# Kernel optimization log

Hardware: AMD Instinct MI355X
Metric: run time of the kernel (lower is better)

The kernel has to match this reference:

```python
import jax, jax.numpy as jnp
import numpy as np

D = 128      # hidden_dim
B = 256      # num graphs in batch
NH = 6144    # head-drug nodes
NT = 6144    # tail-drug nodes
EH = 10240   # head line-graph nodes (edges)
ET = 10240   # tail line-graph nodes (edges)


def _even_batch(n, b):
    # sorted graph assignment with every segment non-empty (PyG Batch invariant)
    return (jnp.arange(n) * b // n).astype(jnp.int32)


def setup_inputs() -> dict:
    key = jax.random.key(0)
    ks = jax.random.split(key, 12)
    w = lambda k: jax.random.normal(k, (D, D), dtype=jnp.float32) * 0.05
    bb = lambda k: jax.random.normal(k, (D,), dtype=jnp.float32) * 0.05
    return {
        "x_node_h": jax.random.normal(ks[0], (NH, D), dtype=jnp.float32),
        "x_node_t": jax.random.normal(ks[1], (NT, D), dtype=jnp.float32),
        "x_line_h": jax.random.normal(ks[2], (EH, D), dtype=jnp.float32),
        "x_line_t": jax.random.normal(ks[3], (ET, D), dtype=jnp.float32),
        "Wh_w": w(ks[4]), "Wh_b": bb(ks[5]),
        "Wt_w": w(ks[6]), "Wt_b": bb(ks[7]),
        "Whl_w": w(ks[8]), "Whl_b": bb(ks[9]),
        "Wtl_w": w(ks[10]), "Wtl_b": bb(ks[11]),
        "h_batch": _even_batch(NH, B),
        "t_batch": _even_batch(NT, B),
        "h_ebatch": _even_batch(EH, B),
        "t_ebatch": _even_batch(ET, B),
        "num_graphs": B,
    }


def _seg_softmax(v, seg, num_segments):
    m = jax.ops.segment_max(v, seg, num_segments=num_segments)
    e = jnp.exp(v - m[seg])
    s = jax.ops.segment_sum(e, seg, num_segments=num_segments)
    return e / s[seg]


def _seg_count(seg, num_segments, dtype):
    c = jax.ops.segment_sum(jnp.ones_like(seg, dtype=dtype), seg, num_segments=num_segments)
    return jnp.maximum(c, 1)


def _mutual_attn(xh, xt, Wh_w, Wh_b, Wt_w, Wt_b, bh, bt, num_graphs):
    lin = lambda x, W, b: x @ W.T + b
    xh1 = lin(xh, Wh_w, Wh_b)
    xt1 = lin(xt, Wt_w, Wt_b)
    xt2 = lin(xt, Wh_w, Wh_b)
    xh2 = lin(xh, Wt_w, Wt_b)
    # (x_t2 @ x_h2^T)^T == x_h2 @ x_t2^T
    alpha = jnp.tanh(xh1 @ xt1.T + xh2 @ xt2.T)  # [Nh, Nt]
    cnt_h = _seg_count(bh, num_graphs, alpha.dtype)
    cnt_t = _seg_count(bt, num_graphs, alpha.dtype)
    # global_mean_pool over rows, then diag of [t_batch]-gather == per-column gather
    pooled_rows = jax.ops.segment_sum(alpha, bh, num_segments=num_graphs) / cnt_h[:, None]  # [B, Nt]
    b_t = pooled_rows[bt, jnp.arange(xt.shape[0])]  # [Nt]
    p_t = _seg_softmax(b_t, bt, num_graphs)
    s_t = jax.ops.segment_sum(p_t[:, None] * xt, bt, num_segments=num_graphs)  # [B, D]
    pooled_cols = jax.ops.segment_sum(alpha.T, bt, num_segments=num_graphs) / cnt_t[:, None]  # [B, Nh]
    b_h = pooled_cols[bh, jnp.arange(xh.shape[0])]  # [Nh]
    p_h = _seg_softmax(b_h, bh, num_graphs)
    s_h = jax.ops.segment_sum(p_h[:, None] * xh, bh, num_segments=num_graphs)  # [B, D]
    return s_h, s_t


def reference(x_node_h, x_node_t, x_line_h, x_line_t,
              Wh_w, Wh_b, Wt_w, Wt_b, Whl_w, Whl_b, Wtl_w, Wtl_b,
              h_batch, t_batch, h_ebatch, t_ebatch, num_graphs):
    s_h, s_t = _mutual_attn(x_node_h, x_node_t, Wh_w, Wh_b, Wt_w, Wt_b,
                            h_batch, t_batch, num_graphs)
    s_h_line, s_t_line = _mutual_attn(x_line_h, x_line_t, Whl_w, Whl_b, Wtl_w, Wtl_b,
                                      h_ebatch, t_ebatch, num_graphs)
    return (s_h, s_t, s_h_line, s_t_line)
```

## Files before the change

### kernel.cpp

```cpp
#include <hip/hip_runtime.h>
#include <math.h>

#define D 128

typedef float f32x4 __attribute__((ext_vector_type(4)));
typedef _Float16 f16x8 __attribute__((ext_vector_type(8)));

union PK4 { _Float16 h[4]; ushort4 v; };

__device__ __forceinline__ f16x8 cvt8(float4 a, float4 b) {
    f16x8 r;
    r[0] = (_Float16)a.x; r[1] = (_Float16)a.y; r[2] = (_Float16)a.z; r[3] = (_Float16)a.w;
    r[4] = (_Float16)b.x; r[5] = (_Float16)b.y; r[6] = (_Float16)b.z; r[7] = (_Float16)b.w;
    return r;
}

__device__ __forceinline__ float tanh_fast(float x) {
    float cx = fminf(fmaxf(x, -15.f), 15.f);
    float t = __expf(2.f * cx);
    return __fdividef(t - 1.f, t + 1.f);
}

template <int LEVEL>
__device__ __forceinline__ void body(
    int g, const float* __restrict__ xh, const float* __restrict__ xt,
    const float* __restrict__ WH, const float* __restrict__ WT,
    const float* __restrict__ bH, const float* __restrict__ bT,
    float* __restrict__ osh, float* __restrict__ ost,
    _Float16* GH, _Float16* GT, _Float16* XH, _Float16* XT,
    float* colpart, float* bh_s, float* pt_s, float* ph_s)
{
    constexpr int R = LEVEL ? 40 : 24;
    constexpr int TM = LEVEL ? 3 : 2;
    constexpr int PAD = TM * 16;
    constexpr float invR = 1.f / (float)R;

    const int tid = threadIdx.x;
    const int w = tid >> 6, l = tid & 63;
    const int lm = l & 15, lq = l >> 4;
    const int base = g * R;
    const int tile0 = 2 * w;

    f16x8 wf[4][4];
#pragma unroll
    for (int ks = 0; ks < 4; ++ks) {
        const int k0 = ks * 32 + lq * 8;
#pragma unroll
        for (int t = 0; t < 2; ++t) {
            const float* p1 = WH + ((tile0 + t) * 16 + lm) * D + k0;
            wf[t][ks] = cvt8(*reinterpret_cast<const float4*>(p1),
                             *reinterpret_cast<const float4*>(p1 + 4));
            const float* p2 = WT + ((tile0 + t) * 16 + lm) * D + k0;
            wf[2 + t][ks] = cvt8(*reinterpret_cast<const float4*>(p2),
                                 *reinterpret_cast<const float4*>(p2 + 4));
        }
    }

    {
        constexpr int UNITS = 2 * PAD * 32;
        for (int u = tid; u < UNITS; u += 256) {
            const int arr = (u >= PAD * 32);
            const int rem = arr ? (u - PAD * 32) : u;
            const int r = rem >> 5, c4 = rem & 31;
            _Float16* Xs = arr ? XT : XH;
            PK4 pk;
            if (r < R) {
                const float* xs = arr ? xt : xh;
                float4 v = *reinterpret_cast<const float4*>(&xs[(base + r) * D + c4 * 4]);
                pk.h[0] = (_Float16)v.x; pk.h[1] = (_Float16)v.y;
                pk.h[2] = (_Float16)v.z; pk.h[3] = (_Float16)v.w;
            } else {
                pk.v = make_ushort4(0, 0, 0, 0);
            }
            *reinterpret_cast<ushort4*>(&Xs[r * 128 + ((c4 * 4) ^ ((r & 7) << 3))]) = pk.v;
        }
        constexpr int GZ = 2 * (PAD - R) * 64;
        for (int u = tid; u < GZ; u += 256) {
            const int arr = (u >= (PAD - R) * 64);
            const int rem = arr ? (u - (PAD - R) * 64) : u;
            const int r = R + (rem >> 6), c4 = rem & 63;
            _Float16* Gs = arr ? GT : GH;
            *reinterpret_cast<ushort4*>(&Gs[r * 256 + c4 * 4]) = make_ushort4(0, 0, 0, 0);
        }
    }
    __syncthreads();

#pragma unroll
    for (int side = 0; side < 2; ++side) {
        const _Float16* Xs = side ? XT : XH;
        const float* __restrict__ bA = side ? bT : bH;
        const float* __restrict__ bB = side ? bH : bT;
        _Float16* Gs = side ? GT : GH;

        f32x4 acc[TM][4];
#pragma unroll
        for (int ti = 0; ti < TM; ++ti)
#pragma unroll
            for (int c2 = 0; c2 < 4; ++c2) acc[ti][c2] = (f32x4){0.f, 0.f, 0.f, 0.f};

#pragma unroll
        for (int ks = 0; ks < 4; ++ks) {
            const int k0 = ks * 32 + lq * 8;
            const int kx = k0 ^ ((lm & 7) << 3);
            f16x8 q[TM];
#pragma unroll
            for (int ti = 0; ti < TM; ++ti)
                q[ti] = *reinterpret_cast<const f16x8*>(&Xs[(ti * 16 + lm) * 128 + kx]);
#pragma unroll
            for (int c2 = 0; c2 < 4; ++c2) {
                const int wfidx = side ? (c2 ^ 2) : c2;
#pragma unroll
                for (int ti = 0; ti < TM; ++ti)
                    acc[ti][c2] = __builtin_amdgcn_mfma_f32_16x16x32_f16(
                        wf[wfidx][ks], q[ti], acc[ti][c2], 0, 0, 0);
            }
        }

#pragma unroll
        for (int c2 = 0; c2 < 4; ++c2) {
            const int ctl = (c2 < 2) ? (tile0 + c2) : (8 + tile0 + (c2 - 2));
            const int nc = ctl * 16 + lq * 4;
            const float* bp = (ctl < 8) ? (bA + nc) : (bB + nc - 128);
            float4 b4 = *reinterpret_cast<const float4*>(bp);
#pragma unroll
            for (int ti = 0; ti < TM; ++ti) {
                int i = ti * 16 + lm;
                if (i < R) {
                    PK4 pk;
                    pk.h[0] = (_Float16)(acc[ti][c2][0] + b4.x);
                    pk.h[1] = (_Float16)(acc[ti][c2][1] + b4.y);
                    pk.h[2] = (_Float16)(acc[ti][c2][2] + b4.z);
                    pk.h[3] = (_Float16)(acc[ti][c2][3] + b4.w);
                    *reinterpret_cast<ushort4*>(&Gs[i * 256 + (nc ^ ((i & 7) << 3))]) = pk.v;
                }
            }
        }
    }
    __syncthreads();

    float cs[3] = {0.f, 0.f, 0.f};
    if (w < TM) {
        f32x4 acc2[TM];
#pragma unroll
        for (int tj = 0; tj < TM; ++tj) acc2[tj] = (f32x4){0.f, 0.f, 0.f, 0.f};

        const int ri = w * 16 + lm;
#pragma unroll
        for (int ksa = 0; ksa < 8; ++ksa) {
            const int k0 = ksa * 32 + lq * 8;
            const int kx = k0 ^ ((lm & 7) << 3);
            f16x8 A = *reinterpret_cast<const f16x8*>(&GH[ri * 256 + kx]);
#pragma unroll
            for (int tj = 0; tj < TM; ++tj) {
                f16x8 B = *reinterpret_cast<const f16x8*>(&GT[(tj * 16 + lm) * 256 + kx]);
                acc2[tj] = __builtin_amdgcn_mfma_f32_16x16x32_f16(A, B, acc2[tj], 0, 0, 0);
            }
        }

        float at[TM][4];
#pragma unroll
        for (int tj = 0; tj < TM; ++tj)
#pragma unroll
            for (int r = 0; r < 4; ++r) at[tj][r] = tanh_fast(acc2[tj][r]);

#pragma unroll
        for (int r = 0; r < 4; ++r) {
            float s = 0.f;
#pragma unroll
            for (int tj = 0; tj < TM; ++tj) s += at[tj][r];
            s += __shfl_xor(s, 1, 64);
            s += __shfl_xor(s, 2, 64);
            s += __shfl_xor(s, 4, 64);
            s += __shfl_xor(s, 8, 64);
            if (lm == 0) bh_s[w * 16 + lq * 4 + r] = s;
        }
#pragma unroll
        for (int tj = 0; tj < TM; ++tj) {
            float s = 0.f;
#pragma unroll
            for (int r = 0; r < 4; ++r) s += at[tj][r];
            s += __shfl_xor(s, 16, 64);
            s += __shfl_xor(s, 32, 64);
            cs[tj] = s;
        }
    }
#pragma unroll
    for (int tj = 0; tj < 3; ++tj)
        if (lq == 0) colpart[w * 48 + tj * 16 + lm] = (tj < TM) ? cs[tj] : 0.f;
    __syncthreads();

    if (w == 0) {
        float v = (l < 48) ? (colpart[l] + colpart[48 + l] + colpart[96 + l] + colpart[144 + l]) : 0.f;
        float val = (l < R) ? v * invR : -INFINITY;
        float m = val;
        for (int o = 32; o; o >>= 1) m = fmaxf(m, __shfl_xor(m, o, 64));
        float e = (l < R) ? __expf(val - m) : 0.f;
        float s = e;
        for (int o = 32; o; o >>= 1) s += __shfl_xor(s, o, 64);
        if (l < R) pt_s[l] = e / s;
    } else if (w == 1) {
        float val = (l < R) ? bh_s[l] * invR : -INFINITY;
        float m = val;
        for (int o = 32; o; o >>= 1) m = fmaxf(m, __shfl_xor(m, o, 64));
        float e = (l < R) ? __expf(val - m) : 0.f;
        float s = e;
        for (int o = 32; o; o >>= 1) s += __shfl_xor(s, o, 64);
        if (l < R) ph_s[l] = e / s;
    }
    __syncthreads();

    if (tid < 128) {
        const int c = tid;
        float a = 0.f;
        for (int j = 0; j < R; ++j)
            a += pt_s[j] * (float)XT[j * 128 + (c ^ ((j & 7) << 3))];
        ost[g * D + c] = a;
    } else {
        const int c = tid - 128;
        float a = 0.f;
        for (int i = 0; i < R; ++i)
            a += ph_s[i] * (float)XH[i * 128 + (c ^ ((i & 7) << 3))];
        osh[g * D + c] = a;
    }
}

__global__ __launch_bounds__(256, 2) void fused_kernel(
    const float* __restrict__ xnh, const float* __restrict__ xnt,
    const float* __restrict__ xlh, const float* __restrict__ xlt,
    const float* __restrict__ Wh, const float* __restrict__ bh,
    const float* __restrict__ Wt, const float* __restrict__ bt,
    const float* __restrict__ Whl, const float* __restrict__ bhl,
    const float* __restrict__ Wtl, const float* __restrict__ btl,
    float* __restrict__ out)
{
    __shared__ __align__(16) _Float16 GH[48 * 256];
    __shared__ __align__(16) _Float16 GT[48 * 256];
    __shared__ __align__(16) _Float16 XH[48 * 128];
    __shared__ __align__(16) _Float16 XT[48 * 128];
    __shared__ float colpart[192], bh_s[48], pt_s[48], ph_s[48];

    int idx = blockIdx.x;
    if (idx < 256)
        body<0>(idx, xnh, xnt, Wh, Wt, bh, bt, out + 0, out + 32768,
                GH, GT, XH, XT, colpart, bh_s, pt_s, ph_s);
    else
        body<1>(idx - 256, xlh, xlt, Whl, Wtl, bhl, btl, out + 65536, out + 98304,
                GH, GT, XH, XT, colpart, bh_s, pt_s, ph_s);
}

extern "C" void kernel_launch(void* const* d_in, const int* in_sizes, int n_in,
                              void* d_out, int out_size, void* d_ws, size_t ws_size,
                              hipStream_t stream) {
    const float* xnh   = (const float*)d_in[0];
    const float* xnt   = (const float*)d_in[1];
    const float* xlh   = (const float*)d_in[2];
    const float* xlt   = (const float*)d_in[3];
    const float* Wh_w  = (const float*)d_in[4];
    const float* Wh_b  = (const float*)d_in[5];
    const float* Wt_w  = (const float*)d_in[6];
    const float* Wt_b  = (const float*)d_in[7];
    const float* Whl_w = (const float*)d_in[8];
    const float* Whl_b = (const float*)d_in[9];
    const float* Wtl_w = (const float*)d_in[10];
    const float* Wtl_b = (const float*)d_in[11];

    float* out = (float*)d_out;

    fused_kernel<<<512, 256, 0, stream>>>(xnh, xnt, xlh, xlt,
                                          Wh_w, Wh_b, Wt_w, Wt_b,
                                          Whl_w, Whl_b, Wtl_w, Wtl_b, out);
}
```

Baseline: 21.76 us.

## Fold the two bilinear projections into one precomputed weight-product matrix

```diff
diff --git a/kernel.cpp b/kernel.cpp
--- a/kernel.cpp
+++ b/kernel.cpp
@@ -7,13 +7,6 @@
 typedef _Float16 f16x8 __attribute__((ext_vector_type(8)));
 
 union PK4 { _Float16 h[4]; ushort4 v; };
-
-__device__ __forceinline__ f16x8 cvt8(float4 a, float4 b) {
-    f16x8 r;
-    r[0] = (_Float16)a.x; r[1] = (_Float16)a.y; r[2] = (_Float16)a.z; r[3] = (_Float16)a.w;
-    r[4] = (_Float16)b.x; r[5] = (_Float16)b.y; r[6] = (_Float16)b.z; r[7] = (_Float16)b.w;
-    return r;
-}
 
 __device__ __forceinline__ float tanh_fast(float x) {
     float cx = fminf(fmaxf(x, -15.f), 15.f);
@@ -21,14 +14,52 @@
     return __fdividef(t - 1.f, t + 1.f);
 }
 
+__global__ __launch_bounds__(256) void prep_M(
+    const float* __restrict__ Wh, const float* __restrict__ Wt,
+    const float* __restrict__ Whl, const float* __restrict__ Wtl,
+    const float* __restrict__ bh, const float* __restrict__ bt,
+    const float* __restrict__ bhl, const float* __restrict__ btl,
+    _Float16* __restrict__ M16, float* __restrict__ aux)
+{
+    const int bid = blockIdx.x, tid = threadIdx.x;
+    const int level = bid >> 6;
+    const float* __restrict__ WH = level ? Whl : Wh;
+    const float* __restrict__ WT = level ? Wtl : Wt;
+    const int b = tid & 127;
+    const int a = (bid & 63) * 2 + (tid >> 7);
+    _Float16* M = M16 + level * 16384;
+
+    float s = 0.f;
+#pragma unroll 4
+    for (int k = 0; k < 128; ++k) {
+        s += WH[k * 128 + a] * WT[k * 128 + b] + WT[k * 128 + a] * WH[k * 128 + b];
+    }
+    M[a * 128 + b] = (_Float16)s;
+
+    if ((bid & 63) == 0) {
+        const float* BH = level ? bhl : bh;
+        const float* BT = level ? btl : bt;
+        if (tid < 128) {
+            float t = 0.f;
+#pragma unroll 4
+            for (int k = 0; k < 128; ++k)
+                t += WH[k * 128 + tid] * BT[k] + WT[k * 128 + tid] * BH[k];
+            aux[level * 128 + tid] = t;
+        } else if (tid == 128) {
+            float c = 0.f;
+            for (int k = 0; k < 128; ++k) c += BH[k] * BT[k];
+            aux[256 + level] = 2.f * c;
+        }
+    }
+}
+
 template <int LEVEL>
 __device__ __forceinline__ void body(
     int g, const float* __restrict__ xh, const float* __restrict__ xt,
-    const float* __restrict__ WH, const float* __restrict__ WT,
-    const float* __restrict__ bH, const float* __restrict__ bT,
+    const _Float16* __restrict__ M16, const float* __restrict__ aux,
     float* __restrict__ osh, float* __restrict__ ost,
-    _Float16* GH, _Float16* GT, _Float16* XH, _Float16* XT,
-    float* colpart, float* bh_s, float* pt_s, float* ph_s)
+    _Float16* Ylds, _Float16* XH, _Float16* XT,
+    float* u_s, float* v_s, float* colpart, float* bh_s, float* pt_s, float* ph_s)
 {
     constexpr int R = LEVEL ? 40 : 24;
     constexpr int TM = LEVEL ? 3 : 2;
@@ -39,21 +70,18 @@
     const int w = tid >> 6, l = tid & 63;
     const int lm = l & 15, lq = l >> 4;
     const int base = g * R;
-    const int tile0 = 2 * w;
-
-    f16x8 wf[4][4];
+
+    const _Float16* __restrict__ M = M16 + LEVEL * 16384;
+    const float* __restrict__ w0 = aux + LEVEL * 128;
+    const float c0 = aux[256 + LEVEL];
+
+    f16x8 mf[2][4];
 #pragma unroll
     for (int ks = 0; ks < 4; ++ks) {
         const int k0 = ks * 32 + lq * 8;
 #pragma unroll
-        for (int t = 0; t < 2; ++t) {
-            const float* p1 = WH + ((tile0 + t) * 16 + lm) * D + k0;
-            wf[t][ks] = cvt8(*reinterpret_cast<const float4*>(p1),
-                             *reinterpret_cast<const float4*>(p1 + 4));
-            const float* p2 = WT + ((tile0 + t) * 16 + lm) * D + k0;
-            wf[2 + t][ks] = cvt8(*reinterpret_cast<const float4*>(p2),
-                                 *reinterpret_cast<const float4*>(p2 + 4));
-        }
+        for (int c2 = 0; c2 < 2; ++c2)
+            mf[c2][ks] = *reinterpret_cast<const f16x8*>(M + ((w * 2 + c2) * 16 + lm) * 128 + k0);
     }
 
     {
@@ -64,75 +92,63 @@
             const int r = rem >> 5, c4 = rem & 31;
             _Float16* Xs = arr ? XT : XH;
             PK4 pk;
+            float part = 0.f;
             if (r < R) {
                 const float* xs = arr ? xt : xh;
                 float4 v = *reinterpret_cast<const float4*>(&xs[(base + r) * D + c4 * 4]);
+                float4 wv = *reinterpret_cast<const float4*>(&w0[c4 * 4]);
+                part = v.x * wv.x + v.y * wv.y + v.z * wv.z + v.w * wv.w;
                 pk.h[0] = (_Float16)v.x; pk.h[1] = (_Float16)v.y;
                 pk.h[2] = (_Float16)v.z; pk.h[3] = (_Float16)v.w;
             } else {
                 pk.v = make_ushort4(0, 0, 0, 0);
             }
             *reinterpret_cast<ushort4*>(&Xs[r * 128 + ((c4 * 4) ^ ((r & 7) << 3))]) = pk.v;
-        }
-        constexpr int GZ = 2 * (PAD - R) * 64;
-        for (int u = tid; u < GZ; u += 256) {
-            const int arr = (u >= (PAD - R) * 64);
-            const int rem = arr ? (u - (PAD - R) * 64) : u;
-            const int r = R + (rem >> 6), c4 = rem & 63;
-            _Float16* Gs = arr ? GT : GH;
-            *reinterpret_cast<ushort4*>(&Gs[r * 256 + c4 * 4]) = make_ushort4(0, 0, 0, 0);
-        }
-    }
-    __syncthreads();
-
-#pragma unroll
-    for (int side = 0; side < 2; ++side) {
-        const _Float16* Xs = side ? XT : XH;
-        const float* __restrict__ bA = side ? bT : bH;
-        const float* __restrict__ bB = side ? bH : bT;
-        _Float16* Gs = side ? GT : GH;
-
-        f32x4 acc[TM][4];
+            part += __shfl_xor(part, 1, 64);
+            part += __shfl_xor(part, 2, 64);
+            part += __shfl_xor(part, 4, 64);
+            part += __shfl_xor(part, 8, 64);
+            part += __shfl_xor(part, 16, 64);
+            if (c4 == 0) (arr ? v_s : u_s)[r] = part;
+        }
+    }
+    __syncthreads();
+
+    f32x4 acc[TM][2];
+#pragma unroll
+    for (int ti = 0; ti < TM; ++ti)
+#pragma unroll
+        for (int c2 = 0; c2 < 2; ++c2) acc[ti][c2] = (f32x4){0.f, 0.f, 0.f, 0.f};
+
+#pragma unroll
+    for (int ks = 0; ks < 4; ++ks) {
+        const int k0 = ks * 32 + lq * 8;
+        const int kx = k0 ^ ((lm & 7) << 3);
+        f16x8 q[TM];
 #pragma unroll
         for (int ti = 0; ti < TM; ++ti)
-#pragma unroll
-            for (int c2 = 0; c2 < 4; ++c2) acc[ti][c2] = (f32x4){0.f, 0.f, 0.f, 0.f};
-
-#pragma unroll
-        for (int ks = 0; ks < 4; ++ks) {
-            const int k0 = ks * 32 + lq * 8;
-            const int kx = k0 ^ ((lm & 7) << 3);
-            f16x8 q[TM];
+            q[ti] = *reinterpret_cast<const f16x8*>(&XH[(ti * 16 + lm) * 128 + kx]);
+#pragma unroll
+        for (int c2 = 0; c2 < 2; ++c2)
 #pragma unroll
             for (int ti = 0; ti < TM; ++ti)
-                q[ti] = *reinterpret_cast<const f16x8*>(&Xs[(ti * 16 + lm) * 128 + kx]);
-#pragma unroll
-            for (int c2 = 0; c2 < 4; ++c2) {
-                const int wfidx = side ? (c2 ^ 2) : c2;
-#pragma unroll
-                for (int ti = 0; ti < TM; ++ti)
-                    acc[ti][c2] = __builtin_amdgcn_mfma_f32_16x16x32_f16(
-                        wf[wfidx][ks], q[ti], acc[ti][c2], 0, 0, 0);
-            }
-        }
-
-#pragma unroll
-        for (int c2 = 0; c2 < 4; ++c2) {
-            const int ctl = (c2 < 2) ? (tile0 + c2) : (8 + tile0 + (c2 - 2));
-            const int nc = ctl * 16 + lq * 4;
-            const float* bp = (ctl < 8) ? (bA + nc) : (bB + nc - 128);
-            float4 b4 = *reinterpret_cast<const float4*>(bp);
-#pragma unroll
-            for (int ti = 0; ti < TM; ++ti) {
-                int i = ti * 16 + lm;
-                if (i < R) {
-                    PK4 pk;
-                    pk.h[0] = (_Float16)(acc[ti][c2][0] + b4.x);
-                    pk.h[1] = (_Float16)(acc[ti][c2][1] + b4.y);
-                    pk.h[2] = (_Float16)(acc[ti][c2][2] + b4.z);
-                    pk.h[3] = (_Float16)(acc[ti][c2][3] + b4.w);
-                    *reinterpret_cast<ushort4*>(&Gs[i * 256 + (nc ^ ((i & 7) << 3))]) = pk.v;
-                }
+                acc[ti][c2] = __builtin_amdgcn_mfma_f32_16x16x32_f16(
+                    mf[c2][ks], q[ti], acc[ti][c2], 0, 0, 0);
+    }
+
+#pragma unroll
+    for (int c2 = 0; c2 < 2; ++c2) {
+        const int nc = (w * 2 + c2) * 16 + lq * 4;
+#pragma unroll
+        for (int ti = 0; ti < TM; ++ti) {
+            int i = ti * 16 + lm;
+            if (i < R) {
+                PK4 pk;
+                pk.h[0] = (_Float16)acc[ti][c2][0];
+                pk.h[1] = (_Float16)acc[ti][c2][1];
+                pk.h[2] = (_Float16)acc[ti][c2][2];
+                pk.h[3] = (_Float16)acc[ti][c2][3];
+                *reinterpret_cast<ushort4*>(&Ylds[i * 128 + (nc ^ ((i & 7) << 3))]) = pk.v;
             }
         }
     }
@@ -144,24 +160,33 @@
 #pragma unroll
         for (int tj = 0; tj < TM; ++tj) acc2[tj] = (f32x4){0.f, 0.f, 0.f, 0.f};
 
-        const int ri = w * 16 + lm;
-#pragma unroll
-        for (int ksa = 0; ksa < 8; ++ksa) {
+#pragma unroll
+        for (int ksa = 0; ksa < 4; ++ksa) {
             const int k0 = ksa * 32 + lq * 8;
             const int kx = k0 ^ ((lm & 7) << 3);
-            f16x8 A = *reinterpret_cast<const f16x8*>(&GH[ri * 256 + kx]);
+            f16x8 A = *reinterpret_cast<const f16x8*>(&Ylds[(w * 16 + lm) * 128 + kx]);
 #pragma unroll
             for (int tj = 0; tj < TM; ++tj) {
-                f16x8 B = *reinterpret_cast<const f16x8*>(&GT[(tj * 16 + lm) * 256 + kx]);
+                f16x8 B = *reinterpret_cast<const f16x8*>(&XT[(tj * 16 + lm) * 128 + kx]);
                 acc2[tj] = __builtin_amdgcn_mfma_f32_16x16x32_f16(A, B, acc2[tj], 0, 0, 0);
             }
         }
 
         float at[TM][4];
 #pragma unroll
-        for (int tj = 0; tj < TM; ++tj)
-#pragma unroll
-            for (int r = 0; r < 4; ++r) at[tj][r] = tanh_fast(acc2[tj][r]);
+        for (int tj = 0; tj < TM; ++tj) {
+            int j = tj * 16 + lm;
+            bool vj = (j < R);
+            float vjv = v_s[vj ? j : 0];
+#pragma unroll
+            for (int r = 0; r < 4; ++r) {
+                int i = w * 16 + lq * 4 + r;
+                bool vi = (i < R);
+                float uiv = u_s[vi ? i : 0];
+                float sv = acc2[tj][r] + uiv + vjv + c0;
+                at[tj][r] = (vi && vj) ? tanh_fast(sv) : 0.f;
+            }
+        }
 
 #pragma unroll
         for (int r = 0; r < 4; ++r) {
@@ -224,28 +249,24 @@
     }
 }
 
-__global__ __launch_bounds__(256, 2) void fused_kernel(
+__global__ __launch_bounds__(256, 4) void fused_kernel(
     const float* __restrict__ xnh, const float* __restrict__ xnt,
     const float* __restrict__ xlh, const float* __restrict__ xlt,
-    const float* __restrict__ Wh, const float* __restrict__ bh,
-    const float* __restrict__ Wt, const float* __restrict__ bt,
-    const float* __restrict__ Whl, const float* __restrict__ bhl,
-    const float* __restrict__ Wtl, const float* __restrict__ btl,
+    const _Float16* __restrict__ M16, const float* __restrict__ aux,
     float* __restrict__ out)
 {
-    __shared__ __align__(16) _Float16 GH[48 * 256];
-    __shared__ __align__(16) _Float16 GT[48 * 256];
+    __shared__ __align__(16) _Float16 Ylds[48 * 128];
     __shared__ __align__(16) _Float16 XH[48 * 128];
     __shared__ __align__(16) _Float16 XT[48 * 128];
-    __shared__ float colpart[192], bh_s[48], pt_s[48], ph_s[48];
+    __shared__ float u_s[48], v_s[48], colpart[192], bh_s[48], pt_s[48], ph_s[48];
 
     int idx = blockIdx.x;
     if (idx < 256)
-        body<0>(idx, xnh, xnt, Wh, Wt, bh, bt, out + 0, out + 32768,
-                GH, GT, XH, XT, colpart, bh_s, pt_s, ph_s);
+        body<0>(idx, xnh, xnt, M16, aux, out + 0, out + 32768,
+                Ylds, XH, XT, u_s, v_s, colpart, bh_s, pt_s, ph_s);
     else
-        body<1>(idx - 256, xlh, xlt, Whl, Wtl, bhl, btl, out + 65536, out + 98304,
-                GH, GT, XH, XT, colpart, bh_s, pt_s, ph_s);
+        body<1>(idx - 256, xlh, xlt, M16, aux, out + 65536, out + 98304,
+                Ylds, XH, XT, u_s, v_s, colpart, bh_s, pt_s, ph_s);
 }
 
 extern "C" void kernel_launch(void* const* d_in, const int* in_sizes, int n_in,
@@ -264,9 +285,11 @@
     const float* Wtl_w = (const float*)d_in[10];
     const float* Wtl_b = (const float*)d_in[11];
 
+    _Float16* M16 = (_Float16*)d_ws;
+    float* aux = (float*)((char*)d_ws + 65536);
     float* out = (float*)d_out;
 
-    fused_kernel<<<512, 256, 0, stream>>>(xnh, xnt, xlh, xlt,
-                                          Wh_w, Wh_b, Wt_w, Wt_b,
-                                          Whl_w, Whl_b, Wtl_w, Wtl_b, out);
-}
+    prep_M<<<128, 256, 0, stream>>>(Wh_w, Wt_w, Whl_w, Wtl_w,
+                                    Wh_b, Wt_b, Whl_b, Wtl_b, M16, aux);
+    fused_kernel<<<512, 256, 0, stream>>>(xnh, xnt, xlh, xlt, M16, aux, out);
+}
```

Measured after the change: 29.34 us. 1.35x slower.
